# Optimization experiments

Measured on AMD Instinct MI355X. Metric: run time of the kernel, lower is better.

Reference implementation:

```python
import jax, jax.numpy as jnp
import numpy as np
import math

D_MODEL = 1024
NUM_HEADS = 16
HEAD_DIM = D_MODEL // NUM_HEADS
CLAMP = 1e9


def setup_inputs() -> dict:
    key = jax.random.key(0)
    k1, k2, k3, k4, k5 = jax.random.split(key, 5)
    B, S = 2, 2048
    x = jax.random.normal(k1, (B, S, D_MODEL), dtype=jnp.float32)
    # torch Linear params, stored as [in, out] (y = x @ W + b)
    s1 = 1.0 / math.sqrt(D_MODEL)
    W_qkv = jax.random.uniform(k2, (D_MODEL, 3 * D_MODEL), jnp.float32, -s1, s1)
    b_qkv = jax.random.uniform(k3, (3 * D_MODEL,), jnp.float32, -s1, s1)
    W_out = jax.random.uniform(k4, (D_MODEL, D_MODEL), jnp.float32, -s1, s1)
    b_out = jax.random.uniform(k5, (D_MODEL,), jnp.float32, -s1, s1)
    return {"x": x, "W_qkv": W_qkv, "b_qkv": b_qkv, "W_out": W_out, "b_out": b_out}


def reference(x, W_qkv, b_qkv, W_out, b_out):
    B, S, D = x.shape
    qkv = x @ W_qkv + b_qkv                       # [B, S, 3*D]
    qkv = qkv.reshape(B, S, NUM_HEADS, 3 * HEAD_DIM).transpose(0, 2, 1, 3)  # [B, H, S, 3*hd]
    q, k, v = jnp.split(qkv, 3, axis=-1)          # each [B, H, S, hd]
    scale = 1.0 / math.sqrt(HEAD_DIM)
    scores = jnp.einsum('bhqd,bhkd->bhqk', q, k) * scale  # [B, H, S, S]
    causal = jnp.tril(jnp.ones((S, S), dtype=bool))
    scores = jnp.where(causal, scores, -jnp.inf)
    scores = jnp.clip(scores, -CLAMP, CLAMP)      # -inf -> -1e9, matching torch clamp
    attn = jax.nn.softmax(scores, axis=-1)
    values = jnp.einsum('bhqk,bhkd->bhqd', attn, v)        # [B, H, S, hd]
    values = values.transpose(0, 2, 1, 3).reshape(B, S, D)  # [B, S, D]
    out = values @ W_out + b_out
    # dropout is identity in eval mode
    return out
```

## Files before the change

kernel.cpp:

```cpp
#include <hip/hip_runtime.h>
#include <hip/hip_bf16.h>

#define D_MODEL 1024
#define NUM_HEADS 16
#define HEAD_DIM 64
#define SEQ 2048
#define BATCH 2
#define ROWS (BATCH * SEQ)

typedef unsigned short u16;
typedef __bf16 bf16x8 __attribute__((ext_vector_type(8)));
typedef float f32x4 __attribute__((ext_vector_type(4)));

__device__ inline u16 f2bfu(float f) {
  unsigned u = __float_as_uint(f);
  unsigned r = (u + 0x7fffu + ((u >> 16) & 1u)) >> 16;
  return (u16)r;
}

__device__ inline unsigned cvt_pk_bf16(float a, float b) {
#if __has_builtin(__builtin_amdgcn_cvt_pk_bf16_f32)
  auto r = __builtin_amdgcn_cvt_pk_bf16_f32(a, b);
  unsigned u;
  __builtin_memcpy(&u, &r, 4);
  return u;
#else
  return (unsigned)f2bfu(a) | ((unsigned)f2bfu(b) << 16);
#endif
}

__device__ inline f32x4 mfma16(bf16x8 a, bf16x8 b, f32x4 c) {
  return __builtin_amdgcn_mfma_f32_16x16x32_bf16(a, b, c, 0, 0, 0);
}

__device__ inline bf16x8 load_frag(const u16* p) {
  union { uint4 v; bf16x8 f; } u;
  u.v = *(const uint4*)p;
  return u.f;
}

__device__ inline void gload_lds16(const u16* g, u16* l) {
  __builtin_amdgcn_global_load_lds((const __attribute__((address_space(1))) void*)g,
                                   (__attribute__((address_space(3))) void*)l, 16, 0, 0);
}


__global__ __launch_bounds__(256) void prep_kernel(const float* __restrict__ x,
                                                   u16* __restrict__ xb,
                                                   const float* __restrict__ Wq,
                                                   u16* __restrict__ WqT,
                                                   const float* __restrict__ Wo,
                                                   u16* __restrict__ WoT) {
  __shared__ float t[32][33];
  const int bid = blockIdx.x;
  if (bid < 4096) {
    int i = bid * 256 + threadIdx.x;
    float4 v = ((const float4*)x)[i];
    uint2 o;
    o.x = cvt_pk_bf16(v.x, v.y);
    o.y = cvt_pk_bf16(v.z, v.w);
    ((uint2*)xb)[i] = o;
    return;
  }
  const float* W;
  u16* Wt;
  int N, tIdx;
  if (bid < 4096 + 3072) { W = Wq; Wt = WqT; N = 3072; tIdx = bid - 4096; }
  else                   { W = Wo; Wt = WoT; N = 1024; tIdx = bid - 7168; }
  const int k0 = (tIdx & 31) * 32, n0 = (tIdx >> 5) * 32;
  const int c = threadIdx.x & 31, r8 = threadIdx.x >> 5;
#pragma unroll
  for (int i = 0; i < 4; i++) {
    int r = r8 + i * 8;
    t[r][c] = W[(size_t)(k0 + r) * N + n0 + c];
  }
  __syncthreads();
#pragma unroll
  for (int i = 0; i < 4; i++) {
    int r = r8 + i * 8;
    Wt[(size_t)(n0 + r) * 1024 + k0 + c] = f2bfu(t[c][r]);
  }
}


__global__ __launch_bounds__(256, 3) void gemm_qkv(const u16* __restrict__ A,
                                                   const u16* __restrict__ Bt,
                                                   const float* __restrict__ bias,
                                                   u16* __restrict__ Qb, u16* __restrict__ Kb,
                                                   u16* __restrict__ Vt) {
  __shared__ u16 lA[3][128 * 32], lB[3][128 * 32];
  const int tid = threadIdx.x;
  const int wave = tid >> 6, lane = tid & 63, ln = lane & 15, quad = lane >> 4;
  const int lin = blockIdx.y * 24 + blockIdx.x;
  const int reg = lin & 7, idx = lin >> 3;
  const int mr = idx / 12, nr = idx - mr * 12;
  const int m0 = ((reg >> 1) * 8 + mr) * 128;
  const int n0 = (((reg & 1) * 12) + nr) * 128;
  const int wm = (wave & 1) * 64, wn = (wave >> 1) * 64;
  f32x4 acc[4][4] = {};

  auto issue = [&](u16* dA, u16* dB, int k0) {
#pragma unroll
    for (int i = 0; i < 2; ++i) {
      int rb = wave * 2 + i;
      gload_lds16(A + (size_t)(m0 + rb * 16 + ln) * 1024 + k0 + quad * 8, dA + rb * 512);
      gload_lds16(Bt + (size_t)(n0 + rb * 16 + ln) * 1024 + k0 + quad * 8, dB + rb * 512);
    }
  };
  auto compute = [&](const u16* sA, const u16* sB) {
    bf16x8 a[4], b[4];
#pragma unroll
    for (int i = 0; i < 4; ++i) {
      a[i] = load_frag(sA + (wm / 16 + i) * 512 + quad * 128 + ln * 8);
      b[i] = load_frag(sB + (wn / 16 + i) * 512 + quad * 128 + ln * 8);
    }
#pragma unroll
    for (int mt = 0; mt < 4; ++mt)
#pragma unroll
      for (int nt = 0; nt < 4; ++nt) acc[mt][nt] = mfma16(a[mt], b[nt], acc[mt][nt]);
  };

  issue(lA[0], lB[0], 0);
  issue(lA[1], lB[1], 32);
  asm volatile("s_waitcnt vmcnt(4)" ::: "memory");
  asm volatile("s_barrier" ::: "memory");

  for (int tt = 0; tt < 10; ++tt) {
    const int t = tt * 3;
    issue(lA[2], lB[2], (t + 2) * 32);
    compute(lA[0], lB[0]);
    asm volatile("s_waitcnt vmcnt(4)" ::: "memory");
    asm volatile("s_barrier" ::: "memory");
    issue(lA[0], lB[0], (t + 3) * 32);
    compute(lA[1], lB[1]);
    asm volatile("s_waitcnt vmcnt(4)" ::: "memory");
    asm volatile("s_barrier" ::: "memory");
    issue(lA[1], lB[1], (t + 4) * 32);
    compute(lA[2], lB[2]);
    asm volatile("s_waitcnt vmcnt(4)" ::: "memory");
    asm volatile("s_barrier" ::: "memory");
  }
  compute(lA[0], lB[0]);
  asm volatile("s_waitcnt vmcnt(0)" ::: "memory");
  asm volatile("s_barrier" ::: "memory");
  compute(lA[1], lB[1]);

#pragma unroll
  for (int mt = 0; mt < 4; ++mt) {
    int row = m0 + wm + mt * 16 + quad * 4;
    int bb = row >> 11, s0 = row & 2047;
#pragma unroll
    for (int nt = 0; nt < 4; ++nt) {
      int col = n0 + wn + nt * 16 + ln;
      float bv = bias[col];
      int h = col / 192, rem = col - h * 192, t3 = rem >> 6, d = rem & 63;
      int bh = bb * NUM_HEADS + h;
      if (t3 == 2) {
        uint2 pk;
        pk.x = cvt_pk_bf16(acc[mt][nt][0] + bv, acc[mt][nt][1] + bv);
        pk.y = cvt_pk_bf16(acc[mt][nt][2] + bv, acc[mt][nt][3] + bv);
        *(uint2*)(Vt + ((size_t)bh * 64 + d) * SEQ + s0) = pk;
      } else {
        u16* dst = (t3 == 0) ? Qb : Kb;
#pragma unroll
        for (int r = 0; r < 4; ++r)
          dst[((size_t)bh * SEQ + s0 + r) * 64 + d] = f2bfu(acc[mt][nt][r] + bv);
      }
    }
  }
}


__global__ __launch_bounds__(512) void attn_kernel(const u16* __restrict__ Qb,
                                                   const u16* __restrict__ Kb,
                                                   const u16* __restrict__ Vt,
                                                   u16* __restrict__ Ob) {
  __shared__ u16 lK[2 * 2 * 64 * 64];
  __shared__ u16 lV[2 * 64 * 64];
  __shared__ u16 lP[8][1152];
  const int tid = threadIdx.x;
  const int wave = tid >> 6, lane = tid & 63;
  const int ln = lane & 15, quad = lane >> 4;
  const int lin = blockIdx.y * 16 + blockIdx.x;
  const int xreg = lin & 7, xidx = lin >> 3;
  const int j = xidx & 15;
  const int bh = xreg * 4 + (xidx >> 4);
  const int lo = j, hi = 31 - j;
  const int myt = (wave < 4) ? lo : hi;
  const int q0w = myt * 64 + (wave & 3) * 16;
  const int sD = myt >> 1;
  const int nsup = (hi + 2) >> 1;
  const u16* Qg = Qb + (size_t)bh * SEQ * 64;
  const u16* Kg = Kb + (size_t)bh * SEQ * 64;
  const u16* Vg = Vt + (size_t)bh * 64 * SEQ;
  u16* lPw = lP[wave];

  bf16x8 qf[2];
#pragma unroll
  for (int ks = 0; ks < 2; ++ks)
    qf[ks] = load_frag(Qg + (size_t)(q0w + ln) * 64 + ks * 32 + quad * 8);

  const u16* sp[4];
  u16* dp[4];
#pragma unroll
  for (int i = 0; i < 4; ++i) {
    if (wave < 4) {
      int c = wave * 4 + i, half = c >> 3, cc = c & 7, rb = cc >> 1, kgh = cc & 1;
      sp[i] = Kg + (size_t)(half * 64 + rb * 16 + ln) * 64 + (kgh * 4 + quad) * 8;
      dp[i] = lK + half * 4096 + rb * 1024 + kgh * 512;
    } else {
      int c2 = wave * 4 - 16 + i, half = c2 >> 3, cc = c2 & 7, rb = cc >> 1, kgh = cc & 1;
      sp[i] = Vg + (size_t)(rb * 16 + ln) * SEQ + half * 64 + (kgh * 4 + quad) * 8;
      dp[i] = lV + half * 4096 + rb * 1024 + kgh * 512;
    }
  }
  if (wave < 4) {
#pragma unroll
    for (int i = 0; i < 4; ++i) gload_lds16(sp[i], dp[i]);
  }

  f32x4 o[4] = {};
  float m_r = -1e30f;
  float l_r = 0.f;
  const float SC = 0.18033688011112042f;
  const int qq = q0w + ln;

  for (int s = 0; s < nsup; ++s) {
    __syncthreads();
    if (wave >= 4) {
#pragma unroll
      for (int i = 0; i < 4; ++i) gload_lds16(sp[i] + (size_t)s * 128, dp[i]);
    }

    if (s <= sD) {
      const u16* lKs = lK + (s & 1) * 8192;
      f32x4 sc[2][4] = {};
      __builtin_amdgcn_s_setprio(1);
#pragma unroll
      for (int h = 0; h < 2; ++h)
#pragma unroll
        for (int mt = 0; mt < 4; ++mt)
#pragma unroll
          for (int ks = 0; ks < 2; ++ks) {
            bf16x8 kf = load_frag(lKs + h * 4096 + mt * 1024 + (ks * 4 + quad) * 128 + ln * 8);
            sc[h][mt] = mfma16(kf, qf[ks], sc[h][mt]);
          }
      __builtin_amdgcn_s_setprio(0);
      if (s == sD) {
#pragma unroll
        for (int h = 0; h < 2; ++h)
#pragma unroll
          for (int mt = 0; mt < 4; ++mt) {
            int key0 = (2 * s + h) * 64 + mt * 16 + quad * 4;
#pragma unroll
            for (int r = 0; r < 4; ++r)
              if (key0 + r > qq) sc[h][mt][r] = -1e30f;
          }
      }
      float mloc = sc[0][0][0];
#pragma unroll
      for (int h = 0; h < 2; ++h)
#pragma unroll
        for (int mt = 0; mt < 4; ++mt)
#pragma unroll
          for (int r = 0; r < 4; ++r) mloc = fmaxf(mloc, sc[h][mt][r]);
      mloc = fmaxf(mloc, __shfl_xor(mloc, 16));
      mloc = fmaxf(mloc, __shfl_xor(mloc, 32));
      if (!__all(mloc - m_r <= 44.0f)) {
        float mnew = fmaxf(m_r, mloc);
        float alpha = __builtin_amdgcn_exp2f((m_r - mnew) * SC);
        l_r *= alpha;
#pragma unroll
        for (int dt = 0; dt < 4; ++dt) o[dt] *= alpha;
        m_r = mnew;
      }
      float nmsc = -m_r * SC;
      float sum = 0.f;
#pragma unroll
      for (int h = 0; h < 2; ++h)
#pragma unroll
        for (int mt = 0; mt < 4; ++mt)
#pragma unroll
          for (int r = 0; r < 4; ++r) {
            float p = __builtin_amdgcn_exp2f(__builtin_fmaf(sc[h][mt][r], SC, nmsc));
            sc[h][mt][r] = p;
            sum += p;
          }
      sum += __shfl_xor(sum, 16);
      sum += __shfl_xor(sum, 32);
      l_r += sum;

      __syncthreads();
      if (wave < 4 && s + 1 < nsup) {
#pragma unroll
        for (int i = 0; i < 4; ++i)
          gload_lds16(sp[i] + (size_t)(s + 1) * (128 * 64), dp[i] + ((s + 1) & 1) * 8192);
      }

#pragma unroll
      for (int h = 0; h < 2; ++h) {
#pragma unroll
        for (int mt = 0; mt < 4; ++mt) {
          uint2 pk;
          pk.x = cvt_pk_bf16(sc[h][mt][0], sc[h][mt][1]);
          pk.y = cvt_pk_bf16(sc[h][mt][2], sc[h][mt][3]);
          int addr = ln * 64 + (((mt * 2 + (quad >> 1)) ^ (ln & 7)) * 8) + (quad & 1) * 4;
          *(uint2*)(lPw + addr) = pk;
        }
        bf16x8 pf[2];
#pragma unroll
        for (int ks = 0; ks < 2; ++ks)
          pf[ks] = load_frag(lPw + ln * 64 + (((ks * 4 + quad) ^ (ln & 7)) * 8));
        __builtin_amdgcn_s_setprio(1);
#pragma unroll
        for (int dt = 0; dt < 4; ++dt)
#pragma unroll
          for (int ks = 0; ks < 2; ++ks) {
            bf16x8 av = load_frag(lV + h * 4096 + dt * 1024 + (ks * 4 + quad) * 128 + ln * 8);
            o[dt] = mfma16(av, pf[ks], o[dt]);
          }
        __builtin_amdgcn_s_setprio(0);
      }
    } else {
      __syncthreads();
      if (wave < 4 && s + 1 < nsup) {
#pragma unroll
        for (int i = 0; i < 4; ++i)
          gload_lds16(sp[i] + (size_t)(s + 1) * (128 * 64), dp[i] + ((s + 1) & 1) * 8192);
      }
    }
  }

  float inv = 1.f / l_r;
#pragma unroll
  for (int dt = 0; dt < 4; ++dt) {
    uint2 pk;
    pk.x = cvt_pk_bf16(o[dt][0] * inv, o[dt][1] * inv);
    pk.y = cvt_pk_bf16(o[dt][2] * inv, o[dt][3] * inv);
    *(uint2*)(lPw + ln * 72 + dt * 16 + quad * 4) = pk;
  }
  const int b = bh >> 4, h2 = bh & 15;
#pragma unroll
  for (int i = 0; i < 2; ++i) {
    int c = lane + i * 64;
    int qq2 = c >> 3, dg = c & 7;
    uint4 val = *(const uint4*)(lPw + qq2 * 72 + dg * 8);
    *(uint4*)(Ob + ((size_t)b * SEQ + q0w + qq2) * 1024 + h2 * 64 + dg * 8) = val;
  }
}


__global__ __launch_bounds__(256, 2) void gemm_out(const u16* __restrict__ A,
                                                   const u16* __restrict__ Bt,
                                                   const float* __restrict__ bias,
                                                   float* __restrict__ out) {
  __shared__ u16 lA[3][128 * 64], lB[3][64 * 64];
  const int tid = threadIdx.x;
  const int wave = tid >> 6, lane = tid & 63, ln = lane & 15, quad = lane >> 4;
  const int lin = blockIdx.y * 16 + blockIdx.x;
  const int reg = lin & 7, idx = lin >> 3;
  const int mr = idx >> 3, nr = idx & 7;
  const int m0 = ((reg >> 1) * 8 + mr) * 128;
  const int n0 = (((reg & 1) * 8) + nr) * 64;
  f32x4 acc[2][4] = {};

  auto issue = [&](u16* dA, u16* dB, int k0) {
#pragma unroll
    for (int i = 0; i < 6; ++i) {
      int c = wave * 6 + i;
      if (c < 16) {
        int kh = c & 1, rb = c >> 1;
        gload_lds16(A + (size_t)(m0 + rb * 16 + ln) * 1024 + k0 + kh * 32 + quad * 8,
                    dA + kh * 4096 + rb * 512);
      } else {
        int c2 = c - 16, kh = c2 & 1, rbn = c2 >> 1;
        gload_lds16(Bt + (size_t)(n0 + rbn * 16 + ln) * 1024 + k0 + kh * 32 + quad * 8,
                    dB + kh * 2048 + rbn * 512);
      }
    }
  };
  auto compute = [&](const u16* sA, const u16* sB) {
    bf16x8 a[2][2], b[4][2];
#pragma unroll
    for (int ks = 0; ks < 2; ++ks) {
#pragma unroll
      for (int i = 0; i < 2; ++i)
        a[i][ks] = load_frag(sA + ks * 4096 + (wave * 2 + i) * 512 + quad * 128 + ln * 8);
#pragma unroll
      for (int i = 0; i < 4; ++i)
        b[i][ks] = load_frag(sB + ks * 2048 + i * 512 + quad * 128 + ln * 8);
    }
#pragma unroll
    for (int ks = 0; ks < 2; ++ks)
#pragma unroll
      for (int mt = 0; mt < 2; ++mt)
#pragma unroll
        for (int nt = 0; nt < 4; ++nt)
          acc[mt][nt] = mfma16(a[mt][ks], b[nt][ks], acc[mt][nt]);
  };

  issue(lA[0], lB[0], 0);
  issue(lA[1], lB[1], 64);
  asm volatile("s_waitcnt vmcnt(6)" ::: "memory");
  asm volatile("s_barrier" ::: "memory");

  for (int tt = 0; tt < 4; ++tt) {
    const int t = tt * 3;
    issue(lA[2], lB[2], (t + 2) * 64);
    compute(lA[0], lB[0]);
    asm volatile("s_waitcnt vmcnt(6)" ::: "memory");
    asm volatile("s_barrier" ::: "memory");
    issue(lA[0], lB[0], (t + 3) * 64);
    compute(lA[1], lB[1]);
    asm volatile("s_waitcnt vmcnt(6)" ::: "memory");
    asm volatile("s_barrier" ::: "memory");
    issue(lA[1], lB[1], (t + 4) * 64);
    compute(lA[2], lB[2]);
    asm volatile("s_waitcnt vmcnt(6)" ::: "memory");
    asm volatile("s_barrier" ::: "memory");
  }
  issue(lA[2], lB[2], 14 * 64);
  compute(lA[0], lB[0]);
  asm volatile("s_waitcnt vmcnt(6)" ::: "memory");
  asm volatile("s_barrier" ::: "memory");
  issue(lA[0], lB[0], 15 * 64);
  compute(lA[1], lB[1]);
  asm volatile("s_waitcnt vmcnt(6)" ::: "memory");
  asm volatile("s_barrier" ::: "memory");
  compute(lA[2], lB[2]);
  asm volatile("s_waitcnt vmcnt(0)" ::: "memory");
  asm volatile("s_barrier" ::: "memory");
  compute(lA[0], lB[0]);

#pragma unroll
  for (int mt = 0; mt < 2; ++mt) {
    int row = m0 + wave * 32 + mt * 16 + quad * 4;
#pragma unroll
    for (int nt = 0; nt < 4; ++nt) {
      int col = n0 + nt * 16 + ln;
      float bv = bias[col];
#pragma unroll
      for (int r = 0; r < 4; ++r)
        out[(size_t)(row + r) * 1024 + col] = acc[mt][nt][r] + bv;
    }
  }
}


extern "C" void kernel_launch(void* const* d_in, const int* in_sizes, int n_in,
                              void* d_out, int out_size, void* d_ws, size_t ws_size,
                              hipStream_t stream) {
  const float* x = (const float*)d_in[0];
  const float* W_qkv = (const float*)d_in[1];
  const float* b_qkv = (const float*)d_in[2];
  const float* W_out = (const float*)d_in[3];
  const float* b_out = (const float*)d_in[4];
  float* out = (float*)d_out;

  char* ws = (char*)d_ws;
  const size_t SZ_XB = (size_t)ROWS * D_MODEL * 2;
  const size_t SZ_WQKVT = (size_t)3 * D_MODEL * D_MODEL * 2;
  const size_t SZ_WOUTT = (size_t)D_MODEL * D_MODEL * 2;
  const size_t SZ_HEADS = (size_t)BATCH * NUM_HEADS * SEQ * HEAD_DIM * 2;
  u16* xb = (u16*)(ws);
  u16* WqkvT = (u16*)(ws + SZ_XB);
  u16* WoutT = (u16*)(ws + SZ_XB + SZ_WQKVT);
  u16* Qb = (u16*)(ws + SZ_XB + SZ_WQKVT + SZ_WOUTT);
  u16* Kb = (u16*)(ws + SZ_XB + SZ_WQKVT + SZ_WOUTT + SZ_HEADS);
  u16* Vt = (u16*)(ws + SZ_XB + SZ_WQKVT + SZ_WOUTT + 2 * SZ_HEADS);
  u16* Ob = (u16*)(ws + SZ_XB + SZ_WQKVT + SZ_WOUTT + 3 * SZ_HEADS);

  prep_kernel<<<dim3(8192), dim3(256), 0, stream>>>(x, xb, W_qkv, WqkvT, W_out, WoutT);
  gemm_qkv<<<dim3(3 * D_MODEL / 128, ROWS / 128), dim3(256), 0, stream>>>(xb, WqkvT, b_qkv,
                                                                          Qb, Kb, Vt);
  attn_kernel<<<dim3(SEQ / 128, BATCH * NUM_HEADS), dim3(512), 0, stream>>>(Qb, Kb, Vt, Ob);
  gemm_out<<<dim3(D_MODEL / 64, ROWS / 128), dim3(256), 0, stream>>>(Ob, WoutT, b_out, out);
}
```

Baseline: 200.7 us.

## Rebalance causal attention work by splitting high tile keys across idle low waves

Waves that own the low query tile previously sat idle once their causal range ended. Now they write out their low-tile result at that point, reload Q for the high tile, and process half of each later key superblock. The two partial softmax states are merged through LDS at the end. This also skips the masked-out half-superblock on diagonal steps. The goal is to remove load imbalance between low and high waves. It costs an extra LDS merge, additional syncs, and more branchy register-heavy code.

```diff
diff --git a/kernel.cpp b/kernel.cpp
--- a/kernel.cpp
+++ b/kernel.cpp
@@ -185,26 +185,30 @@
   const int xreg = lin & 7, xidx = lin >> 3;
   const int j = xidx & 15;
   const int bh = xreg * 4 + (xidx >> 4);
-  const int lo = j, hi = 31 - j;
-  const int myt = (wave < 4) ? lo : hi;
-  const int q0w = myt * 64 + (wave & 3) * 16;
-  const int sD = myt >> 1;
-  const int nsup = (hi + 2) >> 1;
+  const int loT = j, hiT = 31 - j;
+  const int sDlo = loT >> 1, sDhi = hiT >> 1;
+  const int nsup = sDhi + 1;
+  const bool wlo = (wave < 4);
+  const int strip = (wave & 3) * 16;
   const u16* Qg = Qb + (size_t)bh * SEQ * 64;
   const u16* Kg = Kb + (size_t)bh * SEQ * 64;
   const u16* Vg = Vt + (size_t)bh * 64 * SEQ;
   u16* lPw = lP[wave];
-
+  const int b = bh >> 4, h2 = bh & 15;
+  const float SC = 0.18033688011112042f;
+
+  int curq = (wlo ? loT : hiT) * 64 + strip;
+  int qq = curq + ln;
   bf16x8 qf[2];
 #pragma unroll
   for (int ks = 0; ks < 2; ++ks)
-    qf[ks] = load_frag(Qg + (size_t)(q0w + ln) * 64 + ks * 32 + quad * 8);
+    qf[ks] = load_frag(Qg + (size_t)(curq + ln) * 64 + ks * 32 + quad * 8);
 
   const u16* sp[4];
   u16* dp[4];
 #pragma unroll
   for (int i = 0; i < 4; ++i) {
-    if (wave < 4) {
+    if (wlo) {
       int c = wave * 4 + i, half = c >> 3, cc = c & 7, rb = cc >> 1, kgh = cc & 1;
       sp[i] = Kg + (size_t)(half * 64 + rb * 16 + ln) * 64 + (kgh * 4 + quad) * 8;
       dp[i] = lK + half * 4096 + rb * 1024 + kgh * 512;
@@ -214,7 +218,7 @@
       dp[i] = lV + half * 4096 + rb * 1024 + kgh * 512;
     }
   }
-  if (wave < 4) {
+  if (wlo) {
 #pragma unroll
     for (int i = 0; i < 4; ++i) gload_lds16(sp[i], dp[i]);
   }
@@ -222,22 +226,53 @@
   f32x4 o[4] = {};
   float m_r = -1e30f;
   float l_r = 0.f;
-  const float SC = 0.18033688011112042f;
-  const int qq = q0w + ln;
 
   for (int s = 0; s < nsup; ++s) {
     __syncthreads();
-    if (wave >= 4) {
+    if (!wlo) {
 #pragma unroll
       for (int i = 0; i < 4; ++i) gload_lds16(sp[i] + (size_t)s * 128, dp[i]);
     }
 
-    if (s <= sD) {
+    if (wlo && s == sDlo + 1) {
+      float inv = 1.f / l_r;
+#pragma unroll
+      for (int dt = 0; dt < 4; ++dt) {
+        uint2 pk;
+        pk.x = cvt_pk_bf16(o[dt][0] * inv, o[dt][1] * inv);
+        pk.y = cvt_pk_bf16(o[dt][2] * inv, o[dt][3] * inv);
+        *(uint2*)(lPw + ln * 72 + dt * 16 + quad * 4) = pk;
+      }
+#pragma unroll
+      for (int i = 0; i < 2; ++i) {
+        int c = lane + i * 64;
+        int qr = c >> 3, dg = c & 7;
+        uint4 val = *(const uint4*)(lPw + qr * 72 + dg * 8);
+        *(uint4*)(Ob + ((size_t)b * SEQ + curq + qr) * 1024 + h2 * 64 + dg * 8) = val;
+      }
+      m_r = -1e30f;
+      l_r = 0.f;
+#pragma unroll
+      for (int dt = 0; dt < 4; ++dt) o[dt] = (f32x4){0.f, 0.f, 0.f, 0.f};
+      curq = hiT * 64 + strip;
+      qq = curq + ln;
+#pragma unroll
+      for (int ks = 0; ks < 2; ++ks)
+        qf[ks] = load_frag(Qg + (size_t)(curq + ln) * 64 + ks * 32 + quad * 8);
+    }
+
+    const bool two = (s <= sDlo);
+    const int myT = (two && wlo) ? loT : hiT;
+    int hm = two ? 3 : (wlo ? 2 : 1);
+    if (s == (myT >> 1) && !(myT & 1)) hm &= 1;
+
+    f32x4 sc[2][4] = {};
+    if (hm) {
       const u16* lKs = lK + (s & 1) * 8192;
-      f32x4 sc[2][4] = {};
       __builtin_amdgcn_s_setprio(1);
 #pragma unroll
-      for (int h = 0; h < 2; ++h)
+      for (int h = 0; h < 2; ++h) {
+        if (!((hm >> h) & 1)) continue;
 #pragma unroll
         for (int mt = 0; mt < 4; ++mt)
 #pragma unroll
@@ -245,10 +280,12 @@
             bf16x8 kf = load_frag(lKs + h * 4096 + mt * 1024 + (ks * 4 + quad) * 128 + ln * 8);
             sc[h][mt] = mfma16(kf, qf[ks], sc[h][mt]);
           }
+      }
       __builtin_amdgcn_s_setprio(0);
-      if (s == sD) {
-#pragma unroll
-        for (int h = 0; h < 2; ++h)
+      if (s == (myT >> 1)) {
+#pragma unroll
+        for (int h = 0; h < 2; ++h) {
+          if (!((hm >> h) & 1)) continue;
 #pragma unroll
           for (int mt = 0; mt < 4; ++mt) {
             int key0 = (2 * s + h) * 64 + mt * 16 + quad * 4;
@@ -256,14 +293,17 @@
             for (int r = 0; r < 4; ++r)
               if (key0 + r > qq) sc[h][mt][r] = -1e30f;
           }
-      }
-      float mloc = sc[0][0][0];
-#pragma unroll
-      for (int h = 0; h < 2; ++h)
+        }
+      }
+      float mloc = -1e30f;
+#pragma unroll
+      for (int h = 0; h < 2; ++h) {
+        if (!((hm >> h) & 1)) continue;
 #pragma unroll
         for (int mt = 0; mt < 4; ++mt)
 #pragma unroll
           for (int r = 0; r < 4; ++r) mloc = fmaxf(mloc, sc[h][mt][r]);
+      }
       mloc = fmaxf(mloc, __shfl_xor(mloc, 16));
       mloc = fmaxf(mloc, __shfl_xor(mloc, 32));
       if (!__all(mloc - m_r <= 44.0f)) {
@@ -277,7 +317,8 @@
       float nmsc = -m_r * SC;
       float sum = 0.f;
 #pragma unroll
-      for (int h = 0; h < 2; ++h)
+      for (int h = 0; h < 2; ++h) {
+        if (!((hm >> h) & 1)) continue;
 #pragma unroll
         for (int mt = 0; mt < 4; ++mt)
 #pragma unroll
@@ -286,19 +327,23 @@
             sc[h][mt][r] = p;
             sum += p;
           }
+      }
       sum += __shfl_xor(sum, 16);
       sum += __shfl_xor(sum, 32);
       l_r += sum;
-
-      __syncthreads();
-      if (wave < 4 && s + 1 < nsup) {
-#pragma unroll
-        for (int i = 0; i < 4; ++i)
-          gload_lds16(sp[i] + (size_t)(s + 1) * (128 * 64), dp[i] + ((s + 1) & 1) * 8192);
-      }
-
+    }
+
+    __syncthreads();
+    if (wlo && s + 1 < nsup) {
+#pragma unroll
+      for (int i = 0; i < 4; ++i)
+        gload_lds16(sp[i] + (size_t)(s + 1) * (128 * 64), dp[i] + ((s + 1) & 1) * 8192);
+    }
+
+    if (hm) {
 #pragma unroll
       for (int h = 0; h < 2; ++h) {
+        if (!((hm >> h) & 1)) continue;
 #pragma unroll
         for (int mt = 0; mt < 4; ++mt) {
           uint2 pk;
@@ -321,31 +366,46 @@
           }
         __builtin_amdgcn_s_setprio(0);
       }
-    } else {
-      __syncthreads();
-      if (wave < 4 && s + 1 < nsup) {
-#pragma unroll
-        for (int i = 0; i < 4; ++i)
-          gload_lds16(sp[i] + (size_t)(s + 1) * (128 * 64), dp[i] + ((s + 1) & 1) * 8192);
-      }
-    }
-  }
-
-  float inv = 1.f / l_r;
-#pragma unroll
-  for (int dt = 0; dt < 4; ++dt) {
-    uint2 pk;
-    pk.x = cvt_pk_bf16(o[dt][0] * inv, o[dt][1] * inv);
-    pk.y = cvt_pk_bf16(o[dt][2] * inv, o[dt][3] * inv);
-    *(uint2*)(lPw + ln * 72 + dt * 16 + quad * 4) = pk;
-  }
-  const int b = bh >> 4, h2 = bh & 15;
-#pragma unroll
-  for (int i = 0; i < 2; ++i) {
-    int c = lane + i * 64;
-    int qq2 = c >> 3, dg = c & 7;
-    uint4 val = *(const uint4*)(lPw + qq2 * 72 + dg * 8);
-    *(uint4*)(Ob + ((size_t)b * SEQ + q0w + qq2) * 1024 + h2 * 64 + dg * 8) = val;
+    }
+  }
+
+  __syncthreads();
+  if (wlo) {
+    float* fp = (float*)lK + wave * 1152 + lane * 18;
+#pragma unroll
+    for (int dt = 0; dt < 4; ++dt)
+#pragma unroll
+      for (int r = 0; r < 4; ++r) fp[dt * 4 + r] = o[dt][r];
+    fp[16] = m_r;
+    fp[17] = l_r;
+  }
+  __syncthreads();
+  if (!wlo) {
+    const float* fp = (const float*)lK + (wave - 4) * 1152 + lane * 18;
+    float mB = fp[16], lB = fp[17];
+    float mN = fmaxf(m_r, mB);
+    float aA = __builtin_amdgcn_exp2f((m_r - mN) * SC);
+    float aB = __builtin_amdgcn_exp2f((mB - mN) * SC);
+    l_r = l_r * aA + lB * aB;
+#pragma unroll
+    for (int dt = 0; dt < 4; ++dt)
+#pragma unroll
+      for (int r = 0; r < 4; ++r) o[dt][r] = o[dt][r] * aA + fp[dt * 4 + r] * aB;
+    float inv = 1.f / l_r;
+#pragma unroll
+    for (int dt = 0; dt < 4; ++dt) {
+      uint2 pk;
+      pk.x = cvt_pk_bf16(o[dt][0] * inv, o[dt][1] * inv);
+      pk.y = cvt_pk_bf16(o[dt][2] * inv, o[dt][3] * inv);
+      *(uint2*)(lPw + ln * 72 + dt * 16 + quad * 4) = pk;
+    }
+#pragma unroll
+    for (int i = 0; i < 2; ++i) {
+      int c = lane + i * 64;
+      int qr = c >> 3, dg = c & 7;
+      uint4 val = *(const uint4*)(lPw + qr * 72 + dg * 8);
+      *(uint4*)(Ob + ((size_t)b * SEQ + curq + qr) * 1024 + h2 * 64 + dg * 8) = val;
+    }
   }
 }
 
```

Result: no change. 204.4 us (+1.8%).
